# Performance work log

Measured on AMD Instinct MI355X. Metric: run time of the kernel, lower is better.

## Reference

```python
import jax, jax.numpy as jnp
import numpy as np

I, H = 512, 1024

def setup_inputs() -> dict:
    key = jax.random.key(0)
    ks = jax.random.split(key, 5)
    s_ih = 1.0 / np.sqrt(I)
    s_hh = 1.0 / np.sqrt(H)
    return {
        "x": jax.random.normal(ks[0], (512, 64, I), dtype=jnp.float32),
        "W_ih": jax.random.uniform(ks[1], (4 * H, I), minval=-s_ih, maxval=s_ih, dtype=jnp.float32),
        "b_ih": jax.random.uniform(ks[2], (4 * H,), minval=-s_ih, maxval=s_ih, dtype=jnp.float32),
        "W_hh": jax.random.uniform(ks[3], (4 * H, H), minval=-s_hh, maxval=s_hh, dtype=jnp.float32),
        "b_hh": jax.random.uniform(ks[4], (4 * H,), minval=-s_hh, maxval=s_hh, dtype=jnp.float32),
    }

def _lstm(x, W_ih, b_ih, W_hh, b_hh):
    T, B, _ = x.shape
    Hh = W_hh.shape[1]
    # Precompute input projection for all timesteps: [T, B, 4H]
    x_proj = jnp.einsum("tbi,gi->tbg", x, W_ih) + b_ih + b_hh

    def step(carry, xp):
        h, c = carry
        gates = xp + h @ W_hh.T  # [B, 4H]
        i_g, f_g, g_g, o_g = jnp.split(gates, 4, axis=1)
        i_g = jax.nn.sigmoid(i_g)
        f_g = jax.nn.sigmoid(f_g)
        g_g = jnp.tanh(g_g)
        o_g = jax.nn.sigmoid(o_g)
        c = f_g * c + i_g * g_g
        h = o_g * jnp.tanh(c)
        return (h, c), h

    h0 = jnp.zeros((B, Hh), dtype=x.dtype)
    c0 = jnp.zeros((B, Hh), dtype=x.dtype)
    (hT, cT), out = jax.lax.scan(step, (h0, c0), x_proj)
    return out, (hT, cT)

def reference(x, W_ih, b_ih, W_hh, b_hh):
    out, (hT, cT) = _lstm(x, W_ih, b_ih, W_hh, b_hh)
    return out, hT, cT
```

## Files before the change

kernel.cpp:

```cpp
#include <hip/hip_runtime.h>

#define T_STEPS 512
#define BATCH   64
#define IN      512
#define HID     1024
#define GDIM    4096
#define MROWS   (T_STEPS * BATCH)

typedef __attribute__((ext_vector_type(8))) short bf16x8_t;
typedef __attribute__((ext_vector_type(4))) float f32x4_t;

__device__ __forceinline__ unsigned short f2bf(float f) {
  union { float f; unsigned int u; } v; v.f = f;
  unsigned int r = v.u + 0x7FFFu + ((v.u >> 16) & 1u);
  return (unsigned short)(r >> 16);
}
__device__ __forceinline__ float bf2f(unsigned short u) {
  union { unsigned int u; float f; } v; v.u = ((unsigned int)u) << 16;
  return v.f;
}
__device__ __forceinline__ float sigmoidf_(float x) {
  return 1.0f / (1.0f + __expf(-x));
}
__device__ __forceinline__ float tanhf_(float x) {
  return 1.0f - 2.0f / (__expf(2.0f * x) + 1.0f);
}
__device__ __forceinline__ f32x4_t MFMA_(bf16x8_t a, bf16x8_t b, f32x4_t c) {
  return __builtin_amdgcn_mfma_f32_16x16x32_bf16(a, b, c, 0, 0, 0);
}

__global__ void k_cvt(const float* __restrict__ src, unsigned short* __restrict__ dst, int n) {
  int i = (blockIdx.x * blockDim.x + threadIdx.x) * 4;
  if (i + 3 < n) {
    float4 f = *(const float4*)(src + i);
    ushort4 o;
    o.x = f2bf(f.x); o.y = f2bf(f.y); o.z = f2bf(f.z); o.w = f2bf(f.w);
    *(ushort4*)(dst + i) = o;
  }
}

__global__ void k_bias(const float* __restrict__ a, const float* __restrict__ b,
                       float* __restrict__ o) {
  int i = blockIdx.x * blockDim.x + threadIdx.x;
  if (i < GDIM) o[i] = a[i] + b[i];
}

__global__ __launch_bounds__(256) void k_xproj(
    const float* __restrict__ x,
    const unsigned short* __restrict__ Wih,
    const float* __restrict__ bias,
    unsigned short* __restrict__ xproj)
{
  const int AP = 40;
  __shared__ unsigned short Alds[128 * AP];
  __shared__ unsigned short Blds[128 * AP];
  const int tid = threadIdx.x;
  const int w = tid >> 6, l = tid & 63;
  const int m0 = blockIdx.y * 128, n0 = blockIdx.x * 128;
  const int wm = (w >> 1) * 64, wn = (w & 1) * 64;
  f32x4_t acc[4][4] = {};

  for (int k0 = 0; k0 < IN; k0 += 32) {
    #pragma unroll
    for (int it = 0; it < 2; ++it) {
      int chunk = tid + it * 256;
      int row = chunk >> 2;
      int kc  = (chunk & 3) * 8;
      const float* src = x + (size_t)(m0 + row) * IN + k0 + kc;
      float4 f0 = *(const float4*)(src);
      float4 f1 = *(const float4*)(src + 4);
      union { bf16x8_t v; unsigned short s[8]; } u;
      u.s[0]=f2bf(f0.x); u.s[1]=f2bf(f0.y); u.s[2]=f2bf(f0.z); u.s[3]=f2bf(f0.w);
      u.s[4]=f2bf(f1.x); u.s[5]=f2bf(f1.y); u.s[6]=f2bf(f1.z); u.s[7]=f2bf(f1.w);
      *(bf16x8_t*)&Alds[row * AP + kc] = u.v;
    }
    #pragma unroll
    for (int it = 0; it < 2; ++it) {
      int chunk = tid + it * 256;
      int row = chunk >> 2;
      int kc  = (chunk & 3) * 8;
      *(bf16x8_t*)&Blds[row * AP + kc] =
          *(const bf16x8_t*)(Wih + (size_t)(n0 + row) * IN + k0 + kc);
    }
    __syncthreads();
    bf16x8_t a[4], b[4];
    #pragma unroll
    for (int i = 0; i < 4; ++i)
      a[i] = *(const bf16x8_t*)&Alds[(wm + i * 16 + (l & 15)) * AP + ((l >> 4) * 8)];
    #pragma unroll
    for (int i = 0; i < 4; ++i)
      b[i] = *(const bf16x8_t*)&Blds[(wn + i * 16 + (l & 15)) * AP + ((l >> 4) * 8)];
    #pragma unroll
    for (int mi = 0; mi < 4; ++mi) {
      #pragma unroll
      for (int ni = 0; ni < 4; ++ni)
        acc[mi][ni] = __builtin_amdgcn_mfma_f32_16x16x32_bf16(a[mi], b[ni], acc[mi][ni], 0, 0, 0);
    }
    __syncthreads();
  }
  #pragma unroll
  for (int ni = 0; ni < 4; ++ni) {
    int col = n0 + wn + ni * 16 + (l & 15);
    float bv = bias[col];
    #pragma unroll
    for (int mi = 0; mi < 4; ++mi) {
      int rbase = m0 + wm + mi * 16 + (l >> 4) * 4;
      #pragma unroll
      for (int r = 0; r < 4; ++r)
        xproj[(size_t)(rbase + r) * GDIM + col] = f2bf(acc[mi][ni][r] + bv);
    }
  }
}

__global__ __launch_bounds__(256, 1) void k_lstm_persist(
    const unsigned short* __restrict__ xproj,
    const unsigned short* __restrict__ Whh,
    unsigned short* __restrict__ hbuf0,
    unsigned short* __restrict__ hbuf1,
    float* __restrict__ out,
    float* __restrict__ hT,
    float* __restrict__ cT,
    unsigned int* __restrict__ bar)
{
  __shared__ __align__(16) unsigned short Hlds[16384];
  __shared__ float Glds[4][8][33];

  const int tid = threadIdx.x;
  const int w = tid >> 6, l = tid & 63;
  const int grp  = blockIdx.x >> 5;
  const int slot = blockIdx.x & 31;
  const int b0 = grp * 8, n0 = slot * 32;

  {
    bf16x8_t zv = {0, 0, 0, 0, 0, 0, 0, 0};
    #pragma unroll
    for (int i = 0; i < 8; ++i)
      *(bf16x8_t*)((char*)Hlds + (size_t)(i * 256 + tid) * 16) = zv;
  }
  __syncthreads();

  bf16x8_t wf[64];
  {
    const unsigned short* wp0 =
        Whh + (size_t)((w << 10) + n0 + (l & 15)) * HID + ((l >> 4) * 8);
    const unsigned short* wp1 = wp0 + (size_t)16 * HID;
    #pragma unroll
    for (int ks = 0; ks < 32; ++ks) {
      wf[ks]      = *(const bf16x8_t*)(wp0 + ks * 32);
      wf[32 + ks] = *(const bf16x8_t*)(wp1 + ks * 32);
    }
  }

  const int eb = tid >> 5, en = tid & 31;
  const size_t ci = (size_t)(b0 + eb) * HID + n0 + en;
  float creg = 0.0f;

  const int abase = (l & 15) * 2048 + ((l >> 4) * 16);
  const int amask = (l & 7) << 4;

  unsigned int* const fgrp = bar + grp * 512;

  #pragma unroll 1
  for (int t = 0; t < T_STEPS; ++t) {
    const unsigned short* hc = (t & 1) ? hbuf1 : hbuf0;
    unsigned short*       hn = (t & 1) ? hbuf0 : hbuf1;

    const unsigned short* xpp = xproj + ((size_t)t * BATCH + b0 + eb) * GDIM + n0 + en;
    unsigned short x0 = xpp[0], x1 = xpp[1024], x2 = xpp[2048], x3 = xpp[3072];
    asm volatile("" ::: "memory");

    if (t > 0) {
      if (tid == 0) {
        const unsigned int* f = fgrp + (t - 1);
        while (__hip_atomic_load(f, __ATOMIC_RELAXED, __HIP_MEMORY_SCOPE_AGENT) < 32u)
          __builtin_amdgcn_s_sleep(1);
      }
      __syncthreads();
    }

    {
      const char* hsrc = (const char*)(hc + (size_t)b0 * HID);
      bf16x8_t hv[4];
      #pragma unroll
      for (int i = 0; i < 4; ++i) {
        unsigned long long ap = (unsigned long long)(hsrc + (size_t)(i * 256 + tid) * 16);
        asm volatile("global_load_dwordx4 %0, %1, off sc0 sc1"
                     : "=v"(hv[i]) : "v"(ap) : "memory");
      }
      asm volatile("s_waitcnt vmcnt(0)" ::: "memory");
      __builtin_amdgcn_sched_barrier(0);
      #pragma unroll
      for (int i = 0; i < 4; ++i) {
        int d = (i * 256 + tid) * 16;
        int sd = d ^ (((d >> 11) & 7) << 4);
        *(bf16x8_t*)((char*)Hlds + sd) = hv[i];
      }
    }
    __syncthreads();

    f32x4_t ac0 = {0,0,0,0}, ac1 = {0,0,0,0}, ac2 = {0,0,0,0}, ac3 = {0,0,0,0};
    #pragma unroll
    for (int ks = 0; ks < 32; ks += 2) {
      bf16x8_t a0 = *(const bf16x8_t*)((const char*)Hlds + ((abase + (ks+0)*64) ^ amask));
      bf16x8_t a1 = *(const bf16x8_t*)((const char*)Hlds + ((abase + (ks+1)*64) ^ amask));
      ac0 = MFMA_(a0, wf[ks],          ac0);
      ac1 = MFMA_(a0, wf[32 + ks],     ac1);
      ac2 = MFMA_(a1, wf[ks + 1],      ac2);
      ac3 = MFMA_(a1, wf[32 + ks + 1], ac3);
    }
    f32x4_t s0 = ac0 + ac2;
    f32x4_t s1 = ac1 + ac3;

    if ((l >> 4) < 2) {
      int r0 = (l >> 4) * 4, cc = l & 15;
      #pragma unroll
      for (int j = 0; j < 4; ++j) {
        Glds[w][r0 + j][cc]      = s0[j];
        Glds[w][r0 + j][16 + cc] = s1[j];
      }
    }
    __syncthreads();

    float pre0 = Glds[0][eb][en] + bf2f(x0);
    float pre1 = Glds[1][eb][en] + bf2f(x1);
    float pre2 = Glds[2][eb][en] + bf2f(x2);
    float pre3 = Glds[3][eb][en] + bf2f(x3);
    float ig = sigmoidf_(pre0);
    float fg = sigmoidf_(pre1);
    float gg = tanhf_(pre2);
    float og = sigmoidf_(pre3);
    creg = fg * creg + ig * gg;
    float hv = og * tanhf_(creg);

    if (t == T_STEPS - 1) {
      out[((size_t)t * BATCH + b0 + eb) * HID + n0 + en] = hv;
      hT[ci] = hv;
      cT[ci] = creg;
    } else {
      unsigned short mybf = f2bf(hv);
      unsigned short pbf = (unsigned short)(unsigned int)
          __shfl_xor((int)(unsigned int)mybf, 1, 64);
      if ((l & 1) == 0) {
        unsigned int pk = ((unsigned int)mybf) | (((unsigned int)pbf) << 16);
        __hip_atomic_store((unsigned int*)(hn + ci), pk,
                           __ATOMIC_RELAXED, __HIP_MEMORY_SCOPE_AGENT);
      }
      asm volatile("s_waitcnt vmcnt(0)" ::: "memory");
      __syncthreads();
      if (tid == 0)
        (void)__hip_atomic_fetch_add(fgrp + t, 1u,
                                     __ATOMIC_RELAXED, __HIP_MEMORY_SCOPE_AGENT);
      out[((size_t)t * BATCH + b0 + eb) * HID + n0 + en] = hv;
    }
  }
}

__global__ __launch_bounds__(256) void k_step_fused(
    const unsigned short* __restrict__ hprev,
    unsigned short* __restrict__ hnext,
    float* __restrict__ cstate,
    const unsigned short* __restrict__ Whh,
    const unsigned short* __restrict__ Wih,
    const float* __restrict__ x,
    const float* __restrict__ bias,
    float* __restrict__ out,
    float* __restrict__ hT, float* __restrict__ cT,
    int t, int is_last)
{
  const int RS = 1560;
  const int XB = 1032;
  __shared__ unsigned short Hlds[16 * RS];
  __shared__ float Glds[4][16][17];
  const int tid = threadIdx.x;
  const int w = tid >> 6, l = tid & 63;
  const int bg = blockIdx.x >> 6, hs = blockIdx.x & 63;
  const int b0 = bg * 16, n0 = hs * 16;

  #pragma unroll
  for (int it = 0; it < 8; ++it) {
    int chunk = tid + it * 256;
    int row = chunk >> 7;
    int cc  = (chunk & 127) * 8;
    *(bf16x8_t*)&Hlds[row * RS + cc] =
        *(const bf16x8_t*)(hprev + (size_t)(b0 + row) * HID + cc);
  }
  #pragma unroll
  for (int it = 0; it < 4; ++it) {
    int chunk = tid + it * 256;
    int row = chunk >> 6;
    int cc  = (chunk & 63) * 8;
    const float* src = x + ((size_t)t * BATCH + b0 + row) * IN + cc;
    float4 f0 = *(const float4*)(src);
    float4 f1 = *(const float4*)(src + 4);
    union { bf16x8_t v; unsigned short s[8]; } u;
    u.s[0]=f2bf(f0.x); u.s[1]=f2bf(f0.y); u.s[2]=f2bf(f0.z); u.s[3]=f2bf(f0.w);
    u.s[4]=f2bf(f1.x); u.s[5]=f2bf(f1.y); u.s[6]=f2bf(f1.z); u.s[7]=f2bf(f1.w);
    *(bf16x8_t*)&Hlds[row * RS + XB + cc] = u.v;
  }
  __syncthreads();

  f32x4_t acc = {0.f, 0.f, 0.f, 0.f};
  const int gcol = (w << 10) + n0 + (l & 15);
  const unsigned short* wp = Whh + (size_t)gcol * HID + ((l >> 4) * 8);
  const unsigned short* ap = &Hlds[(l & 15) * RS + ((l >> 4) * 8)];
  #pragma unroll 4
  for (int ks = 0; ks < 32; ++ks) {
    bf16x8_t a = *(const bf16x8_t*)(ap);
    bf16x8_t b = *(const bf16x8_t*)(wp);
    acc = __builtin_amdgcn_mfma_f32_16x16x32_bf16(a, b, acc, 0, 0, 0);
    ap += 32; wp += 32;
  }
  const unsigned short* wpx = Wih + (size_t)gcol * IN + ((l >> 4) * 8);
  const unsigned short* apx = &Hlds[(l & 15) * RS + XB + ((l >> 4) * 8)];
  #pragma unroll 4
  for (int ks = 0; ks < 16; ++ks) {
    bf16x8_t a = *(const bf16x8_t*)(apx);
    bf16x8_t b = *(const bf16x8_t*)(wpx);
    acc = __builtin_amdgcn_mfma_f32_16x16x32_bf16(a, b, acc, 0, 0, 0);
    apx += 32; wpx += 32;
  }

  {
    int r0 = (l >> 4) * 4, cc = l & 15;
    Glds[w][r0 + 0][cc] = acc[0];
    Glds[w][r0 + 1][cc] = acc[1];
    Glds[w][r0 + 2][cc] = acc[2];
    Glds[w][r0 + 3][cc] = acc[3];
  }
  __syncthreads();

  int b = tid >> 4, n = tid & 15;
  float pre[4];
  #pragma unroll
  for (int g = 0; g < 4; ++g)
    pre[g] = Glds[g][b][n] + bias[(g << 10) + n0 + n];
  float ig = sigmoidf_(pre[0]);
  float fg = sigmoidf_(pre[1]);
  float gg = tanhf_(pre[2]);
  float og = sigmoidf_(pre[3]);
  size_t ci = (size_t)(b0 + b) * HID + n0 + n;
  float cn = fg * cstate[ci] + ig * gg;
  float hv = og * tanhf_(cn);
  cstate[ci] = cn;
  out[((size_t)t * BATCH + b0 + b) * HID + n0 + n] = hv;
  hnext[ci] = f2bf(hv);
  if (is_last) { hT[ci] = hv; cT[ci] = cn; }
}

extern "C" void kernel_launch(void* const* d_in, const int* in_sizes, int n_in,
                              void* d_out, int out_size, void* d_ws, size_t ws_size,
                              hipStream_t stream) {
  const float* x    = (const float*)d_in[0];
  const float* Wihf = (const float*)d_in[1];
  const float* bih  = (const float*)d_in[2];
  const float* Whhf = (const float*)d_in[3];
  const float* bhh  = (const float*)d_in[4];
  float* out = (float*)d_out;

  char* ws = (char*)d_ws;
  size_t off = 0;
  auto take = [&](size_t bytes) {
    char* p = ws + off;
    off = (off + bytes + 255) & ~(size_t)255;
    return p;
  };
  unsigned short* wih_b = (unsigned short*)take((size_t)GDIM * IN * 2);
  unsigned short* whh_b = (unsigned short*)take((size_t)GDIM * HID * 2);
  float*          bias  = (float*)take((size_t)GDIM * 4);
  unsigned short* h0    = (unsigned short*)take((size_t)BATCH * HID * 2);
  unsigned short* h1    = (unsigned short*)take((size_t)BATCH * HID * 2);
  float*          cbuf  = (float*)take((size_t)BATCH * HID * 4);
  unsigned int*   bar   = (unsigned int*)take((size_t)8 * 512 * 4);
  unsigned short* xproj = (unsigned short*)take((size_t)MROWS * GDIM * 2);
  size_t full_need = off;
  const int primary = (ws_size >= full_need) ? 1 : 0;
  (void)in_sizes; (void)n_in; (void)out_size;

  k_cvt<<<(GDIM * IN / 4 + 255) / 256, 256, 0, stream>>>(Wihf, wih_b, GDIM * IN);
  k_cvt<<<(GDIM * HID / 4 + 255) / 256, 256, 0, stream>>>(Whhf, whh_b, GDIM * HID);
  k_bias<<<(GDIM + 255) / 256, 256, 0, stream>>>(bih, bhh, bias);
  (void)hipMemsetAsync(h0, 0, (size_t)BATCH * HID * 2, stream);

  float* hT = out + (size_t)T_STEPS * BATCH * HID;
  float* cT = hT + (size_t)BATCH * HID;

  if (primary) {
    (void)hipMemsetAsync(bar, 0, (size_t)8 * 512 * 4, stream);
    k_xproj<<<dim3(GDIM / 128, MROWS / 128), 256, 0, stream>>>(x, wih_b, bias, xproj);
    void* p_xproj = (void*)xproj; void* p_whh = (void*)whh_b;
    void* p_h0 = (void*)h0;       void* p_h1 = (void*)h1;
    void* p_out = (void*)out;     void* p_hT = (void*)hT;
    void* p_cT = (void*)cT;       void* p_fl = (void*)bar;
    void* args[8] = {&p_xproj, &p_whh, &p_h0, &p_h1, &p_out, &p_hT, &p_cT, &p_fl};
    hipError_t err = hipLaunchCooperativeKernel((const void*)k_lstm_persist,
                                                dim3(256), dim3(256), args, 0, stream);
    if (err == hipSuccess) return;
  }

  (void)hipMemsetAsync(cbuf, 0, (size_t)BATCH * HID * 4, stream);
  unsigned short* hp = h0;
  unsigned short* hn = h1;
  for (int t = 0; t < T_STEPS; ++t) {
    int last = (t == T_STEPS - 1) ? 1 : 0;
    k_step_fused<<<256, 256, 0, stream>>>(hp, hn, cbuf, whh_b, wih_b, x, bias,
                                          out, hT, cT, t, last);
    unsigned short* tmp = hp; hp = hn; hn = tmp;
  }
}
```

Measured before the change: 2.041 ms.

## Replace counter barrier with sentinel-polled ring buffer for hidden state

Drops the per-step atomic counter barrier (waitcnt, syncthreads, fetch_add, spin on the flag). Each block now polls the previous step's hidden state directly from a 64-slot ring buffer until no word equals a sentinel. Slots 32 steps ahead are reset to the sentinel as each step is written. This takes the flag round-trip off the serial critical path. In exchange it adds spin-polling on data loads, extra sentinel stores, a large ring memset, and a correctness risk if a real bf16 pair equals the sentinel value or the 32-step reset distance is ever violated.

Result: no change. 2.042 ms (+0.1%).

```diff
diff --git a/kernel.cpp b/kernel.cpp
--- a/kernel.cpp
+++ b/kernel.cpp
@@ -6,6 +6,8 @@
 #define HID     1024
 #define GDIM    4096
 #define MROWS   (T_STEPS * BATCH)
+#define RING    64
+#define SENTW   0x7F7F7F7Fu
 
 typedef __attribute__((ext_vector_type(8))) short bf16x8_t;
 typedef __attribute__((ext_vector_type(4))) float f32x4_t;
@@ -115,12 +117,10 @@
 __global__ __launch_bounds__(256, 1) void k_lstm_persist(
     const unsigned short* __restrict__ xproj,
     const unsigned short* __restrict__ Whh,
-    unsigned short* __restrict__ hbuf0,
-    unsigned short* __restrict__ hbuf1,
+    unsigned short* __restrict__ ring,
     float* __restrict__ out,
     float* __restrict__ hT,
-    float* __restrict__ cT,
-    unsigned int* __restrict__ bar)
+    float* __restrict__ cT)
 {
   __shared__ __align__(16) unsigned short Hlds[16384];
   __shared__ float Glds[4][8][33];
@@ -158,42 +158,40 @@
   const int abase = (l & 15) * 2048 + ((l >> 4) * 16);
   const int amask = (l & 7) << 4;
 
-  unsigned int* const fgrp = bar + grp * 512;
-
   #pragma unroll 1
   for (int t = 0; t < T_STEPS; ++t) {
-    const unsigned short* hc = (t & 1) ? hbuf1 : hbuf0;
-    unsigned short*       hn = (t & 1) ? hbuf0 : hbuf1;
-
     const unsigned short* xpp = xproj + ((size_t)t * BATCH + b0 + eb) * GDIM + n0 + en;
     unsigned short x0 = xpp[0], x1 = xpp[1024], x2 = xpp[2048], x3 = xpp[3072];
     asm volatile("" ::: "memory");
 
     if (t > 0) {
-      if (tid == 0) {
-        const unsigned int* f = fgrp + (t - 1);
-        while (__hip_atomic_load(f, __ATOMIC_RELAXED, __HIP_MEMORY_SCOPE_AGENT) < 32u)
-          __builtin_amdgcn_s_sleep(1);
-      }
-      __syncthreads();
-    }
-
-    {
-      const char* hsrc = (const char*)(hc + (size_t)b0 * HID);
-      bf16x8_t hv[4];
-      #pragma unroll
-      for (int i = 0; i < 4; ++i) {
-        unsigned long long ap = (unsigned long long)(hsrc + (size_t)(i * 256 + tid) * 16);
-        asm volatile("global_load_dwordx4 %0, %1, off sc0 sc1"
-                     : "=v"(hv[i]) : "v"(ap) : "memory");
-      }
-      asm volatile("s_waitcnt vmcnt(0)" ::: "memory");
+      const char* rsrc = (const char*)(ring +
+          ((size_t)((t - 1) & (RING - 1)) * BATCH + b0) * HID);
+      union { bf16x8_t v; unsigned int u[4]; } hv[4];
+      unsigned int need = 1u;
+      do {
+        #pragma unroll
+        for (int i = 0; i < 4; ++i) {
+          unsigned long long ap = (unsigned long long)(rsrc + (size_t)(i * 256 + tid) * 16);
+          asm volatile("global_load_dwordx4 %0, %1, off sc0 sc1"
+                       : "=v"(hv[i].v) : "v"(ap) : "memory");
+        }
+        asm volatile("s_waitcnt vmcnt(0)" ::: "memory");
+        unsigned int bad = 0;
+        #pragma unroll
+        for (int i = 0; i < 4; ++i) {
+          bad |= (hv[i].u[0] == SENTW) | (hv[i].u[1] == SENTW);
+          bad |= (hv[i].u[2] == SENTW) | (hv[i].u[3] == SENTW);
+        }
+        need = bad;
+        if (need) __builtin_amdgcn_s_sleep(1);
+      } while (need);
       __builtin_amdgcn_sched_barrier(0);
       #pragma unroll
       for (int i = 0; i < 4; ++i) {
         int d = (i * 256 + tid) * 16;
         int sd = d ^ (((d >> 11) & 7) << 4);
-        *(bf16x8_t*)((char*)Hlds + sd) = hv[i];
+        *(bf16x8_t*)((char*)Hlds + sd) = hv[i].v;
       }
     }
     __syncthreads();
@@ -242,14 +240,13 @@
           __shfl_xor((int)(unsigned int)mybf, 1, 64);
       if ((l & 1) == 0) {
         unsigned int pk = ((unsigned int)mybf) | (((unsigned int)pbf) << 16);
-        __hip_atomic_store((unsigned int*)(hn + ci), pk,
+        unsigned short* rdst = ring + (size_t)(t & (RING - 1)) * BATCH * HID;
+        __hip_atomic_store((unsigned int*)(rdst + ci), pk,
+                           __ATOMIC_RELAXED, __HIP_MEMORY_SCOPE_AGENT);
+        unsigned short* rrst = ring + (size_t)((t + 32) & (RING - 1)) * BATCH * HID;
+        __hip_atomic_store((unsigned int*)(rrst + ci), SENTW,
                            __ATOMIC_RELAXED, __HIP_MEMORY_SCOPE_AGENT);
       }
-      asm volatile("s_waitcnt vmcnt(0)" ::: "memory");
-      __syncthreads();
-      if (tid == 0)
-        (void)__hip_atomic_fetch_add(fgrp + t, 1u,
-                                     __ATOMIC_RELAXED, __HIP_MEMORY_SCOPE_AGENT);
       out[((size_t)t * BATCH + b0 + eb) * HID + n0 + en] = hv;
     }
   }
@@ -370,7 +367,7 @@
   unsigned short* h0    = (unsigned short*)take((size_t)BATCH * HID * 2);
   unsigned short* h1    = (unsigned short*)take((size_t)BATCH * HID * 2);
   float*          cbuf  = (float*)take((size_t)BATCH * HID * 4);
-  unsigned int*   bar   = (unsigned int*)take((size_t)8 * 512 * 4);
+  unsigned short* ring  = (unsigned short*)take((size_t)RING * BATCH * HID * 2);
   unsigned short* xproj = (unsigned short*)take((size_t)MROWS * GDIM * 2);
   size_t full_need = off;
   const int primary = (ws_size >= full_need) ? 1 : 0;
@@ -385,13 +382,12 @@
   float* cT = hT + (size_t)BATCH * HID;
 
   if (primary) {
-    (void)hipMemsetAsync(bar, 0, (size_t)8 * 512 * 4, stream);
+    (void)hipMemsetAsync(ring, 0x7F, (size_t)RING * BATCH * HID * 2, stream);
     k_xproj<<<dim3(GDIM / 128, MROWS / 128), 256, 0, stream>>>(x, wih_b, bias, xproj);
     void* p_xproj = (void*)xproj; void* p_whh = (void*)whh_b;
-    void* p_h0 = (void*)h0;       void* p_h1 = (void*)h1;
-    void* p_out = (void*)out;     void* p_hT = (void*)hT;
-    void* p_cT = (void*)cT;       void* p_fl = (void*)bar;
-    void* args[8] = {&p_xproj, &p_whh, &p_h0, &p_h1, &p_out, &p_hT, &p_cT, &p_fl};
+    void* p_ring = (void*)ring;   void* p_out = (void*)out;
+    void* p_hT = (void*)hT;       void* p_cT = (void*)cT;
+    void* args[6] = {&p_xproj, &p_whh, &p_ring, &p_out, &p_hT, &p_cT};
     hipError_t err = hipLaunchCooperativeKernel((const void*)k_lstm_persist,
                                                 dim3(256), dim3(256), args, 0, stream);
     if (err == hipSuccess) return;
```
